# Kernel optimization log

Hardware: AMD Instinct MI355X
Metric: run time of the kernel (lower is better)

## Reference

```python
import jax, jax.numpy as jnp
import numpy as np

B, S, D, H, DFF = 8, 1024, 1024, 16, 4096
HD = D // H
EPS_COS = 1e-8
EPS_LN = 1e-5


def setup_inputs() -> dict:
    key = jax.random.key(0)
    ks = jax.random.split(key, 12)
    inp = {
        "x": jax.random.normal(ks[0], (B, S, D), jnp.float32),
        "ln1_w": jnp.ones((D,), jnp.float32),
        "ln1_b": jnp.zeros((D,), jnp.float32),
        "in_proj_w": jax.random.normal(ks[1], (3 * D, D), jnp.float32) * 0.02,
        "in_proj_b": jnp.zeros((3 * D,), jnp.float32),
        "out_proj_w": jax.random.normal(ks[2], (D, D), jnp.float32) * 0.02,
        "out_proj_b": jnp.zeros((D,), jnp.float32),
        "ln2_w": jnp.ones((D,), jnp.float32),
        "ln2_b": jnp.zeros((D,), jnp.float32),
        "mu_weight": jax.random.uniform(ks[3], (DFF, D), jnp.float32, -1.0, 1.0) * (1.0 / np.sqrt(D)),
        "sigma_weight": jax.random.normal(ks[4], (DFF, D), jnp.float32) * 0.02,
        "gate_param": jnp.full((DFF,), 0.1, jnp.float32),
        "mu_bias": jnp.zeros((DFF,), jnp.float32),
        "ffn2_w": jax.random.normal(ks[5], (D, DFF), jnp.float32) * 0.02,
        "ffn2_b": jnp.zeros((D,), jnp.float32),
    }
    return inp


def _layernorm(x, w, b):
    mu = jnp.mean(x, axis=-1, keepdims=True)
    var = jnp.mean(jnp.square(x - mu), axis=-1, keepdims=True)
    return (x - mu) * jax.lax.rsqrt(var + EPS_LN) * w + b


def _mha_causal(h, in_proj_w, in_proj_b, out_proj_w, out_proj_b):
    # h: [B,S,D]; combined qkv projection as in torch nn.MultiheadAttention
    qkv = h @ in_proj_w.T + in_proj_b                      # [B,S,3D]
    q, k, v = jnp.split(qkv, 3, axis=-1)
    def heads(t):
        return t.reshape(B, S, H, HD).transpose(0, 2, 1, 3)  # [B,H,S,HD]
    q, k, v = heads(q), heads(k), heads(v)
    logits = jnp.einsum("bhqd,bhkd->bhqk", q, k) / jnp.sqrt(jnp.float32(HD))
    causal = jnp.tril(jnp.ones((S, S), bool))
    logits = jnp.where(causal, logits, jnp.float32(-jnp.inf))
    attn = jax.nn.softmax(logits, axis=-1)
    o = jnp.einsum("bhqk,bhkd->bhqd", attn, v)
    o = o.transpose(0, 2, 1, 3).reshape(B, S, D)
    return o @ out_proj_w.T + out_proj_b


def _moie_linear(xr, mu_weight, sigma_weight, gate_param, mu_bias):
    # xr: [N,D]. cosine similarity via GEMM + norm reductions (no (N,out,in) blowup)
    keys = mu_weight * jax.nn.softplus(sigma_weight)       # [DFF,D]
    dots = xr @ keys.T                                      # [N,DFF]
    xn = jnp.maximum(jnp.linalg.norm(xr, axis=-1, keepdims=True), EPS_COS)
    kn = jnp.maximum(jnp.linalg.norm(keys, axis=-1), EPS_COS)
    scores = dots / (xn * kn[None, :])                      # [N,DFF]
    weights = jax.nn.relu(scores - gate_param[None, :])
    comp = xr @ mu_weight.T + mu_bias                       # [N,DFF]
    masked = comp * weights
    return masked, scores


def reference(x, ln1_w, ln1_b, in_proj_w, in_proj_b, out_proj_w, out_proj_b,
              ln2_w, ln2_b, mu_weight, sigma_weight, gate_param, mu_bias,
              ffn2_w, ffn2_b):
    h = _layernorm(x, ln1_w, ln1_b)
    attn_out = _mha_causal(h, in_proj_w, in_proj_b, out_proj_w, out_proj_b)
    x = x + attn_out
    ffn_in = _layernorm(x, ln2_w, ln2_b)
    xr = ffn_in.reshape(-1, D)                              # [N,D]
    masked, scores = _moie_linear(xr, mu_weight, sigma_weight, gate_param, mu_bias)
    ffn1_out = masked.reshape(B, S, DFF)
    act = jax.nn.silu(ffn1_out)
    ffn2_out = act @ ffn2_w.T + ffn2_b
    x = x + ffn2_out
    return x, scores, masked
```

## Files before the change

### kernel.cpp

```cpp
#include <hip/hip_runtime.h>

typedef unsigned short u16;
typedef unsigned int u32;
typedef unsigned long long u64;
typedef __attribute__((ext_vector_type(8))) short short8;
typedef __attribute__((ext_vector_type(4))) float f32x4;

#define DEV static __device__ __forceinline__

DEV u16 f2b(float f) {
  union { float f; u32 u; } a; a.f = f;
  u32 r = a.u + 0x7fffu + ((a.u >> 16) & 1u);
  return (u16)(r >> 16);
}

DEV f32x4 mfma16(short8 a, short8 b, f32x4 c) {
  return __builtin_amdgcn_mfma_f32_16x16x32_bf16(a, b, c, 0, 0, 0);
}

DEV void async16(const void* g, void* l) {
  __builtin_amdgcn_global_load_lds(
      (const __attribute__((address_space(1))) u32*)g,
      (__attribute__((address_space(3))) u32*)l, 16, 0, 0);
}

__global__ __launch_bounds__(256) void f2bf4(const float* __restrict__ src,
                                             u16* __restrict__ dst, int n4) {
  const int stride = gridDim.x * 256;
  for (int i = blockIdx.x * 256 + threadIdx.x; i < n4; i += stride) {
    const f32x4 v = ((const f32x4*)src)[i];
    union { u64 q; u16 s[4]; } pk;
    pk.s[0] = f2b(v[0]); pk.s[1] = f2b(v[1]); pk.s[2] = f2b(v[2]); pk.s[3] = f2b(v[3]);
    ((u64*)dst)[i] = pk.q;
  }
}

__global__ __launch_bounds__(256) void prep_keys(
    const float* __restrict__ mu, const float* __restrict__ sg,
    u16* __restrict__ wcat, float* __restrict__ kn) {
  __shared__ float s1[4];
  const int row = blockIdx.x, tid = threadIdx.x, lane = tid & 63, wave = tid >> 6;
  const f32x4 m = *(const f32x4*)(mu + (size_t)row * 1024 + tid * 4);
  const f32x4 s = *(const f32x4*)(sg + (size_t)row * 1024 + tid * 4);
  float q = 0.f;
  union { u64 q; u16 s[4]; } pkk, pkm;
  #pragma unroll
  for (int j = 0; j < 4; ++j) {
    const float sp = (s[j] > 20.f) ? s[j] : log1pf(__expf(s[j]));
    const float k = m[j] * sp;
    q += k * k;
    pkk.s[j] = f2b(k);
    pkm.s[j] = f2b(m[j]);
  }
  *(u64*)(wcat + (size_t)row * 1024 + tid * 4) = pkk.q;
  *(u64*)(wcat + (size_t)(4096 + row) * 1024 + tid * 4) = pkm.q;
  #pragma unroll
  for (int d = 1; d < 64; d <<= 1) q += __shfl_xor(q, d);
  if (lane == 0) s1[wave] = q;
  __syncthreads();
  if (tid == 0) kn[row] = 1.0f / fmaxf(sqrtf(s1[0] + s1[1] + s1[2] + s1[3]), 1e-8f);
}

__global__ __launch_bounds__(256) void ln_kernel(
    const float* __restrict__ x, const float* __restrict__ w,
    const float* __restrict__ b, u16* __restrict__ y, float* __restrict__ xn) {
  __shared__ float s1[4], s2[4];
  const int row = blockIdx.x, tid = threadIdx.x, lane = tid & 63, wave = tid >> 6;
  const f32x4 xv = *(const f32x4*)(x + (size_t)row * 1024 + tid * 4);
  float s = xv[0] + xv[1] + xv[2] + xv[3];
  float q = xv[0]*xv[0] + xv[1]*xv[1] + xv[2]*xv[2] + xv[3]*xv[3];
  #pragma unroll
  for (int d = 1; d < 64; d <<= 1) { s += __shfl_xor(s, d); q += __shfl_xor(q, d); }
  if (lane == 0) { s1[wave] = s; s2[wave] = q; }
  __syncthreads();
  s = s1[0] + s1[1] + s1[2] + s1[3];
  q = s2[0] + s2[1] + s2[2] + s2[3];
  const float mean = s * (1.f / 1024.f);
  const float inv = rsqrtf(q * (1.f / 1024.f) - mean * mean + 1e-5f);
  const f32x4 wv = *(const f32x4*)(w + tid * 4);
  const f32x4 bv = *(const f32x4*)(b + tid * 4);
  float yv[4];
  union { u64 q; u16 s[4]; } pk;
  #pragma unroll
  for (int j = 0; j < 4; ++j) {
    yv[j] = (xv[j] - mean) * inv * wv[j] + bv[j];
    pk.s[j] = f2b(yv[j]);
  }
  *(u64*)(y + (size_t)row * 1024 + tid * 4) = pk.q;
  if (xn) {
    float qs = yv[0]*yv[0] + yv[1]*yv[1] + yv[2]*yv[2] + yv[3]*yv[3];
    #pragma unroll
    for (int d = 1; d < 64; d <<= 1) qs += __shfl_xor(qs, d);
    __syncthreads();
    if (lane == 0) s1[wave] = qs;
    __syncthreads();
    if (tid == 0) xn[row] = 1.0f / fmaxf(sqrtf(s1[0] + s1[1] + s1[2] + s1[3]), 1e-8f);
  }
}

template<int MODE, int BM>
__global__ __launch_bounds__(512, 2) void gemm_bt(
    const u16* __restrict__ A, const u16* __restrict__ W,
    int M, int N, int K,
    const float* __restrict__ aux0, const float* __restrict__ aux1,
    float* __restrict__ fo0,
    u16* __restrict__ bo0, u16* __restrict__ bo1, u16* __restrict__ bo2) {
  constexpr int MF = BM / 32;
  constexpr int A_U16 = BM * 32;
  constexpr int STRIDE = A_U16 + 8192;
  constexpr int AISS = BM / 128;
  constexpr int LPT = AISS + 2;
  __shared__ __align__(16) u16 lds[3 * STRIDE];

  const int tid = threadIdx.x;
  const int lane = tid & 63, wave = tid >> 6;
  const int x = lane & 15, g = lane >> 4;
  const int wm = wave >> 2, wn = wave & 3;

  const int gx = N >> 8;
  const int nwg = gridDim.x;
  const int wg = ((int)blockIdx.x & 7) * (nwg >> 3) + ((int)blockIdx.x >> 3);
  const int by = wg / gx, bx = wg - by * gx;
  const int m0 = by * BM, n0 = bx * 256;

  const u16* srcA[AISS]; const u16* srcB[2];
  int dA[AISS], dB[2];
  #pragma unroll
  for (int i = 0; i < AISS; ++i) {
    const int rp = i * 64 + (tid >> 3);
    const int pre = (tid & 7) ^ (rp & 7);
    const int row = rp * 2 + (pre & 1), col = (pre >> 1) * 8;
    srcA[i] = A + (size_t)(m0 + row) * K + col;
    dA[i] = i * 4096 + tid * 8;
  }
  #pragma unroll
  for (int i = 0; i < 2; ++i) {
    const int rp = i * 64 + (tid >> 3);
    const int pre = (tid & 7) ^ (rp & 7);
    const int row = rp * 2 + (pre & 1), col = (pre >> 1) * 8;
    srcB[i] = W + (size_t)(n0 + row) * K + col;
    dB[i] = A_U16 + i * 4096 + tid * 8;
  }
  const int lane_off = (x >> 1) * 64 + (((2 * g + (x & 1)) ^ (x >> 1)) * 8);
  const int aoff = wm * (BM / 4) * 64 + lane_off;
  const int boff = A_U16 + wn * 2048 + lane_off;

  f32x4 acc[MF][4];
  #pragma unroll
  for (int f = 0; f < MF; ++f)
    #pragma unroll
    for (int j = 0; j < 4; ++j) acc[f][j] = (f32x4){0.f, 0.f, 0.f, 0.f};

  const int NT = K >> 5;
  auto stage = [&](int t, int b) {
    u16* buf = lds + b * STRIDE;
    const size_t ko = (size_t)t * 32;
    #pragma unroll
    for (int i = 0; i < AISS; ++i) async16(srcA[i] + ko, buf + dA[i]);
    #pragma unroll
    for (int i = 0; i < 2; ++i) async16(srcB[i] + ko, buf + dB[i]);
  };
  stage(0, 0);
  stage(1, 1);
  int br = 0, bs = 2;
  for (int t = 0; t < NT; ++t) {
    if (t < NT - 1)
      asm volatile("s_waitcnt vmcnt(%0)\n\ts_barrier" :: "n"(LPT) : "memory");
    else
      asm volatile("s_waitcnt vmcnt(0)\n\ts_barrier" ::: "memory");
    const u16* bufr = lds + br * STRIDE;
    short8 bfr[4], af[MF];
    #pragma unroll
    for (int j = 0; j < 4; ++j) bfr[j] = *(const short8*)(bufr + boff + j * 512);
    #pragma unroll
    for (int f = 0; f < MF; ++f) af[f] = *(const short8*)(bufr + aoff + f * 512);
    if (t + 2 < NT) stage(t + 2, bs);
    __builtin_amdgcn_s_setprio(1);
    #pragma unroll
    for (int f = 0; f < MF; ++f)
      #pragma unroll
      for (int j = 0; j < 4; ++j) acc[f][j] = mfma16(af[f], bfr[j], acc[f][j]);
    __builtin_amdgcn_s_setprio(0);
    br = (br == 2) ? 0 : br + 1;
    bs = (bs == 2) ? 0 : bs + 1;
  }

  const int col_base = n0 + wn * 64;
  const int row_base = m0 + wm * (BM / 2);
  #pragma unroll
  for (int f = 0; f < MF; ++f)
    #pragma unroll
    for (int j = 0; j < 4; ++j)
      #pragma unroll
      for (int r = 0; r < 4; ++r) {
        const int row = row_base + f * 16 + g * 4 + r;
        const int col = col_base + j * 16 + x;
        float v = acc[f][j][r];
        if constexpr (MODE == 0) {
          v += aux0[col];
          const int part = col >> 10, cc = col & 1023;
          const int hh = cc >> 6, dd = cc & 63;
          const size_t idx = ((size_t)((row >> 10) * 16 + hh) * 1024 + (row & 1023)) * 64 + dd;
          if (part == 0) bo0[idx] = f2b(v * 0.125f);
          else if (part == 1) bo1[idx] = f2b(v);
          else bo2[idx] = f2b(v);
        } else {
          fo0[(size_t)row * 1024 + col] = v + aux0[col] + aux1[(size_t)row * 1024 + col];
        }
      }
}

__global__ __launch_bounds__(512, 2) void gemm8p_moie(
    const u16* __restrict__ A, const u16* __restrict__ W,
    const float* __restrict__ xni, const float* __restrict__ kni,
    const float* __restrict__ mub, const float* __restrict__ gate,
    float* __restrict__ oscore, float* __restrict__ omask,
    u16* __restrict__ oact) {
  __shared__ __align__(16) u16 lds[65536];
  const int tid = threadIdx.x;
  const int lane = tid & 63, wave = tid >> 6;
  const int x = lane & 15, g = lane >> 4, h = x >> 1, pp = x & 1;
  const int wm = wave >> 2, wn = wave & 3;

  const int bid = (int)blockIdx.x;
  const int local = bid >> 3;
  const int by = (bid & 7) * 4 + (local & 3);
  const int bx = local >> 2;
  const int m0 = by * 256, n0 = bx * 128;

  const int rp0 = tid >> 3, j0 = tid & 7;
  const int prow = rp0 * 2 + (j0 & 1);
  const int pcol = (((j0 >> 1) ^ (rp0 & 3)) & 3) * 8;
  const u16* hsrc[4];
  hsrc[0] = A + (size_t)(m0 + prow) * 1024 + pcol;
  hsrc[1] = A + (size_t)(m0 + 128 + prow) * 1024 + pcol;
  hsrc[2] = W + (size_t)(n0 + prow) * 1024 + pcol;
  hsrc[3] = W + (size_t)(4096 + n0 + prow) * 1024 + pcol;
  const int dst0 = tid * 8;

  const int laneoff = h * 64 + (((2 * g + pp) ^ ((h & 3) << 1)) * 8);

  f32x4 acc[8][4];
  #pragma unroll
  for (int f = 0; f < 8; ++f)
    #pragma unroll
    for (int j = 0; j < 4; ++j) acc[f][j] = (f32x4){0.f, 0.f, 0.f, 0.f};

  auto stage = [&](int o, int kk, int kt, int b) {
    u16* dst = lds + b * 32768 + o * 16384 + kk * 8192 + dst0;
    const int koff = kt * 64 + kk * 32;
    async16(hsrc[o * 2 + 0] + koff, dst);
    async16(hsrc[o * 2 + 1] + koff, dst + 4096);
  };

  stage(1, 0, 0, 0); stage(0, 0, 0, 0); stage(1, 1, 0, 0); stage(0, 1, 0, 0);
  stage(1, 0, 1, 1); stage(0, 0, 1, 1); stage(1, 1, 1, 1);
  asm volatile("s_waitcnt vmcnt(6)\n\ts_barrier" ::: "memory");

  constexpr int NTK = 16;
  short8 bf[4];
  for (int t = 0; t < NTK; ++t) {
    const int b = t & 1;
    const u16* bufA = lds + b * 32768;
    const u16* bufB = bufA + 16384;
    #pragma unroll
    for (int w = 0; w < 4; ++w) {
      const int kk = w >> 1, fh = w & 1;
      short8 af[4];
      if (fh == 0) {
        #pragma unroll
        for (int j = 0; j < 4; ++j)
          bf[j] = *(const short8*)(bufB + kk * 8192 + wn * 2048 + j * 512 + laneoff);
      }
      #pragma unroll
      for (int f = 0; f < 4; ++f)
        af[f] = *(const short8*)(bufA + kk * 8192 + wm * 4096 + (fh * 4 + f) * 512 + laneoff);
      if (w == 0) { if (t + 1 < NTK) stage(0, 1, t + 1, (t + 1) & 1); }
      else if (t + 2 < NTK) {
        if (w == 1) stage(1, 0, t + 2, b);
        else if (w == 2) stage(0, 0, t + 2, b);
        else stage(1, 1, t + 2, b);
      }
      asm volatile("s_barrier" ::: "memory");
      asm volatile("s_waitcnt lgkmcnt(0)" ::: "memory");
      __builtin_amdgcn_sched_barrier(0);
      __builtin_amdgcn_s_setprio(1);
      #pragma unroll
      for (int f = 0; f < 4; ++f)
        #pragma unroll
        for (int j = 0; j < 4; ++j)
          acc[fh * 4 + f][j] = mfma16(af[f], bf[j], acc[fh * 4 + f][j]);
      __builtin_amdgcn_s_setprio(0);
      if (w == 3 && t + 1 < NTK) {
        if (t + 1 < NTK - 1)
          asm volatile("s_waitcnt vmcnt(6)\n\ts_barrier" ::: "memory");
        else
          asm volatile("s_waitcnt vmcnt(0)\n\ts_barrier" ::: "memory");
      } else {
        asm volatile("s_barrier" ::: "memory");
      }
    }
  }

  __syncthreads();
  float* sl = (float*)lds;
  if (wn < 2) {
    #pragma unroll
    for (int f = 0; f < 8; ++f)
      #pragma unroll
      for (int j = 0; j < 4; ++j) {
        const int lcol = wn * 64 + j * 16 + x;
        const int gcol = n0 + lcol;
        const float kv = kni[gcol];
        #pragma unroll
        for (int r = 0; r < 4; ++r) {
          const int lrow = wm * 128 + f * 16 + g * 4 + r;
          const int grow = m0 + lrow;
          const float s = acc[f][j][r] * xni[grow] * kv;
          sl[lrow * 128 + (lcol ^ (g << 4))] = s;
          oscore[(size_t)grow * 4096 + gcol] = s;
        }
      }
  }
  __syncthreads();
  if (wn >= 2) {
    #pragma unroll
    for (int f = 0; f < 8; ++f)
      #pragma unroll
      for (int j = 0; j < 4; ++j) {
        const int lcol = (wn - 2) * 64 + j * 16 + x;
        const int gcol = n0 + lcol;
        const float gt = gate[gcol], mb = mub[gcol];
        #pragma unroll
        for (int r = 0; r < 4; ++r) {
          const int lrow = wm * 128 + f * 16 + g * 4 + r;
          const int grow = m0 + lrow;
          const float s = sl[lrow * 128 + (lcol ^ (g << 4))];
          const float comp = acc[f][j][r] + mb;
          const float mk = comp * fmaxf(s - gt, 0.f);
          omask[(size_t)grow * 4096 + gcol] = mk;
          oact[(size_t)grow * 4096 + gcol] = f2b(mk / (1.f + __expf(-mk)));
        }
      }
  }
}

__global__ __launch_bounds__(256) void attn_kernel(
    const u16* __restrict__ Q, const u16* __restrict__ Kg,
    const u16* __restrict__ Vg, u16* __restrict__ O) {
  __shared__ __align__(16) u16 Kl[64 * 72];
  __shared__ __align__(16) u16 Vt[64 * 72];
  __shared__ __align__(16) u16 Pl[4][16 * 72];
  const int bh = blockIdx.x;
  const int qt = blockIdx.y;
  const int tid = threadIdx.x, lane = tid & 63, wave = tid >> 6;
  const int x = lane & 15, g = lane >> 4;
  const u16* Qb = Q + (size_t)bh * 1024 * 64;
  const u16* Kb = Kg + (size_t)bh * 1024 * 64;
  const u16* Vb = Vg + (size_t)bh * 1024 * 64;
  const int qbase = qt * 64 + wave * 16;
  const short8 qf0 = *(const short8*)&Qb[(qbase + x) * 64 + g * 8];
  const short8 qf1 = *(const short8*)&Qb[(qbase + x) * 64 + 32 + g * 8];
  float mrun[4], lrun[4];
  f32x4 oacc[4];
  #pragma unroll
  for (int r = 0; r < 4; ++r) { mrun[r] = -1e30f; lrun[r] = 0.f; }
  #pragma unroll
  for (int d = 0; d < 4; ++d) oacc[d] = (f32x4){0.f, 0.f, 0.f, 0.f};

  for (int t = 0; t <= qt; ++t) {
    __syncthreads();
    #pragma unroll
    for (int p = 0; p < 2; ++p) {
      const int s = tid + p * 256;
      const int row = s >> 3, c = s & 7;
      *(short8*)&Kl[row * 72 + c * 8] = *(const short8*)&Kb[(size_t)(t * 64 + row) * 64 + c * 8];
    }
    #pragma unroll
    for (int p = 0; p < 2; ++p) {
      const int kv = (tid >> 3) + p * 32;
      const int d0 = (tid & 7) * 8;
      const short8 v8 = *(const short8*)&Vb[(size_t)(t * 64 + kv) * 64 + d0];
      #pragma unroll
      for (int j = 0; j < 8; ++j) {
        const int d = d0 + j;
        Vt[d * 72 + ((kv + 8 * ((d >> 3) & 7)) & 63)] = (u16)v8[j];
      }
    }
    __syncthreads();

    float sc[4][4];
    #pragma unroll
    for (int nb = 0; nb < 4; ++nb) {
      f32x4 a = (f32x4){0.f, 0.f, 0.f, 0.f};
      const short8 kf0 = *(const short8*)&Kl[(nb * 16 + x) * 72 + g * 8];
      const short8 kf1 = *(const short8*)&Kl[(nb * 16 + x) * 72 + 32 + g * 8];
      a = mfma16(qf0, kf0, a);
      a = mfma16(qf1, kf1, a);
      #pragma unroll
      for (int r = 0; r < 4; ++r) sc[nb][r] = a[r];
    }
    if (t == qt) {
      #pragma unroll
      for (int nb = 0; nb < 4; ++nb)
        #pragma unroll
        for (int r = 0; r < 4; ++r)
          if (t * 64 + nb * 16 + x > qbase + g * 4 + r) sc[nb][r] = -1e30f;
    }
    float mnew[4], psum[4], scl[4];
    #pragma unroll
    for (int r = 0; r < 4; ++r) {
      float mx = fmaxf(fmaxf(sc[0][r], sc[1][r]), fmaxf(sc[2][r], sc[3][r]));
      #pragma unroll
      for (int d = 1; d < 16; d <<= 1) mx = fmaxf(mx, __shfl_xor(mx, d));
      mnew[r] = fmaxf(mrun[r], mx);
      scl[r] = __expf(mrun[r] - mnew[r]);
      mrun[r] = mnew[r];
      psum[r] = 0.f;
    }
    float p[4][4];
    #pragma unroll
    for (int nb = 0; nb < 4; ++nb)
      #pragma unroll
      for (int r = 0; r < 4; ++r) {
        p[nb][r] = __expf(sc[nb][r] - mnew[r]);
        psum[r] += p[nb][r];
      }
    #pragma unroll
    for (int r = 0; r < 4; ++r) {
      #pragma unroll
      for (int d = 1; d < 16; d <<= 1) psum[r] += __shfl_xor(psum[r], d);
      lrun[r] = lrun[r] * scl[r] + psum[r];
      #pragma unroll
      for (int db = 0; db < 4; ++db) oacc[db][r] *= scl[r];
    }
    u16* Pw = Pl[wave];
    #pragma unroll
    for (int nb = 0; nb < 4; ++nb)
      #pragma unroll
      for (int r = 0; r < 4; ++r)
        Pw[(g * 4 + r) * 72 + nb * 16 + x] = f2b(p[nb][r]);
    const short8 pf0 = *(const short8*)&Pw[x * 72 + g * 8];
    const short8 pf1 = *(const short8*)&Pw[x * 72 + 32 + g * 8];
    #pragma unroll
    for (int db = 0; db < 4; ++db) {
      const int d = db * 16 + x;
      const int swz = 8 * ((d >> 3) & 7);
      const short8 vf0 = *(const short8*)&Vt[d * 72 + ((g * 8 + swz) & 63)];
      const short8 vf1 = *(const short8*)&Vt[d * 72 + ((g * 8 + 32 + swz) & 63)];
      oacc[db] = mfma16(pf0, vf0, oacc[db]);
      oacc[db] = mfma16(pf1, vf1, oacc[db]);
    }
  }
  const int b = bh >> 4, hh = bh & 15;
  #pragma unroll
  for (int db = 0; db < 4; ++db)
    #pragma unroll
    for (int r = 0; r < 4; ++r) {
      const int qrow = qbase + g * 4 + r;
      O[((size_t)(b * 1024 + qrow)) * 1024 + hh * 64 + db * 16 + x] = f2b(oacc[db][r] / lrun[r]);
    }
}

extern "C" void kernel_launch(void* const* d_in, const int* in_sizes, int n_in,
                              void* d_out, int out_size, void* d_ws, size_t ws_size,
                              hipStream_t stream) {
  const float* x    = (const float*)d_in[0];
  const float* ln1w = (const float*)d_in[1];
  const float* ln1b = (const float*)d_in[2];
  const float* wip  = (const float*)d_in[3];
  const float* bip  = (const float*)d_in[4];
  const float* wop  = (const float*)d_in[5];
  const float* bop  = (const float*)d_in[6];
  const float* ln2w = (const float*)d_in[7];
  const float* ln2b = (const float*)d_in[8];
  const float* muw  = (const float*)d_in[9];
  const float* sgw  = (const float*)d_in[10];
  const float* gate = (const float*)d_in[11];
  const float* mub  = (const float*)d_in[12];
  const float* wf2  = (const float*)d_in[13];
  const float* bf2  = (const float*)d_in[14];

  float* out_x = (float*)d_out;
  float* out_scores = out_x + (size_t)8192 * 1024;
  float* out_masked = out_scores + (size_t)8192 * 4096;

  char* ws = (char*)d_ws;
  size_t off = 0;
  auto alloc = [&](size_t n) { char* p = ws + off; off += (n + 255) & ~(size_t)255; return p; };
  u16* h_bf    = (u16*)alloc((size_t)8192 * 1024 * 2);
  u16* q_bf    = (u16*)alloc((size_t)8192 * 1024 * 2);
  u16* k_bf    = (u16*)alloc((size_t)8192 * 1024 * 2);
  u16* v_bf    = (u16*)alloc((size_t)8192 * 1024 * 2);
  u16* o_bf    = (u16*)alloc((size_t)8192 * 1024 * 2);
  float* x_res = (float*)alloc((size_t)8192 * 1024 * 4);
  u16* xr_bf   = (u16*)alloc((size_t)8192 * 1024 * 2);
  float* xn    = (float*)alloc((size_t)8192 * 4);
  float* kn    = (float*)alloc((size_t)4096 * 4);
  u16* wcat    = (u16*)alloc((size_t)8192 * 1024 * 2);
  u16* wip_b   = (u16*)alloc((size_t)3072 * 1024 * 2);
  u16* wop_b   = (u16*)alloc((size_t)1024 * 1024 * 2);
  u16* wf2_b   = (u16*)alloc((size_t)1024 * 4096 * 2);
  u16* act_bf  = (u16*)alloc((size_t)8192 * 4096 * 2);

  f2bf4<<<1024, 256, 0, stream>>>(wip, wip_b, 3072 * 1024 / 4);
  f2bf4<<<512, 256, 0, stream>>>(wop, wop_b, 1024 * 1024 / 4);
  f2bf4<<<1024, 256, 0, stream>>>(wf2, wf2_b, 1024 * 4096 / 4);
  prep_keys<<<4096, 256, 0, stream>>>(muw, sgw, wcat, kn);
  ln_kernel<<<8192, 256, 0, stream>>>(x, ln1w, ln1b, h_bf, nullptr);
  gemm_bt<0, 256><<<384, 512, 0, stream>>>(h_bf, wip_b, 8192, 3072, 1024,
      bip, nullptr, nullptr, q_bf, k_bf, v_bf);
  attn_kernel<<<dim3(128, 16), 256, 0, stream>>>(q_bf, k_bf, v_bf, o_bf);
  gemm_bt<1, 128><<<256, 512, 0, stream>>>(o_bf, wop_b, 8192, 1024, 1024,
      bop, x, x_res, nullptr, nullptr, nullptr);
  ln_kernel<<<8192, 256, 0, stream>>>(x_res, ln2w, ln2b, xr_bf, xn);
  gemm8p_moie<<<1024, 512, 0, stream>>>(xr_bf, wcat, xn, kn, mub, gate,
      out_scores, out_masked, act_bf);
  gemm_bt<3, 128><<<256, 512, 0, stream>>>(act_bf, wf2_b, 8192, 1024, 4096,
      bf2, x_res, out_x, nullptr, nullptr, nullptr);
}
```

Before: 598.2 us.

## Interleave key/mu weight rows per wave and deepen MOIE GEMM pipeline

The fused MOIE GEMM now loads B rows so that key and mu_weight rows for the same output column sit in the same wave's fragments: each 64-row chunk holds 32 key rows followed by 32 mu rows. This lets every wave compute score, mask and SiLU directly from its own registers, removing the LDS round trip and the two __syncthreads in the epilogue. The K loop also moves from a 2-buffer, 64-wide stage to a 4-buffer, 32-wide stage ring with three stages in flight, which adds barriers per k-step but gives more latency hiding.

```diff
diff --git a/kernel.cpp b/kernel.cpp
--- a/kernel.cpp
+++ b/kernel.cpp
@@ -210,13 +210,13 @@
       }
 }
 
-__global__ __launch_bounds__(512, 2) void gemm8p_moie(
+__global__ __launch_bounds__(512, 2) void moie_gemm(
     const u16* __restrict__ A, const u16* __restrict__ W,
     const float* __restrict__ xni, const float* __restrict__ kni,
     const float* __restrict__ mub, const float* __restrict__ gate,
     float* __restrict__ oscore, float* __restrict__ omask,
     u16* __restrict__ oact) {
-  __shared__ __align__(16) u16 lds[65536];
+  __shared__ __align__(16) u16 lds[4 * 16384];
   const int tid = threadIdx.x;
   const int lane = tid & 63, wave = tid >> 6;
   const int x = lane & 15, g = lane >> 4, h = x >> 1, pp = x & 1;
@@ -231,117 +231,96 @@
   const int rp0 = tid >> 3, j0 = tid & 7;
   const int prow = rp0 * 2 + (j0 & 1);
   const int pcol = (((j0 >> 1) ^ (rp0 & 3)) & 3) * 8;
-  const u16* hsrc[4];
-  hsrc[0] = A + (size_t)(m0 + prow) * 1024 + pcol;
-  hsrc[1] = A + (size_t)(m0 + 128 + prow) * 1024 + pcol;
-  hsrc[2] = W + (size_t)(n0 + prow) * 1024 + pcol;
-  hsrc[3] = W + (size_t)(4096 + n0 + prow) * 1024 + pcol;
+  const u16* Asrc[2]; const u16* Bsrc[2];
+  Asrc[0] = A + (size_t)(m0 + prow) * 1024 + pcol;
+  Asrc[1] = A + (size_t)(m0 + 128 + prow) * 1024 + pcol;
+  #pragma unroll
+  for (int c = 0; c < 2; ++c) {
+    const int rb = c * 128 + prow;
+    const u16* base = (rb & 32) ? (W + (size_t)4096 * 1024) : W;
+    Bsrc[c] = base + (size_t)(n0 + ((rb >> 6) << 5) + (rb & 31)) * 1024 + pcol;
+  }
   const int dst0 = tid * 8;
-
   const int laneoff = h * 64 + (((2 * g + pp) ^ ((h & 3) << 1)) * 8);
 
   f32x4 acc[8][4];
   #pragma unroll
-  for (int f = 0; f < 8; ++f)
-    #pragma unroll
-    for (int j = 0; j < 4; ++j) acc[f][j] = (f32x4){0.f, 0.f, 0.f, 0.f};
-
-  auto stage = [&](int o, int kk, int kt, int b) {
-    u16* dst = lds + b * 32768 + o * 16384 + kk * 8192 + dst0;
-    const int koff = kt * 64 + kk * 32;
-    async16(hsrc[o * 2 + 0] + koff, dst);
-    async16(hsrc[o * 2 + 1] + koff, dst + 4096);
+  for (int i = 0; i < 8; ++i)
+    #pragma unroll
+    for (int j = 0; j < 4; ++j) acc[i][j] = (f32x4){0.f, 0.f, 0.f, 0.f};
+
+  auto stageA = [&](int t) {
+    u16* dst = lds + (t & 3) * 16384 + dst0;
+    const int ko = t * 32;
+    async16(Asrc[0] + ko, dst);
+    async16(Asrc[1] + ko, dst + 4096);
   };
-
-  stage(1, 0, 0, 0); stage(0, 0, 0, 0); stage(1, 1, 0, 0); stage(0, 1, 0, 0);
-  stage(1, 0, 1, 1); stage(0, 0, 1, 1); stage(1, 1, 1, 1);
-  asm volatile("s_waitcnt vmcnt(6)\n\ts_barrier" ::: "memory");
-
-  constexpr int NTK = 16;
-  short8 bf[4];
-  for (int t = 0; t < NTK; ++t) {
-    const int b = t & 1;
-    const u16* bufA = lds + b * 32768;
-    const u16* bufB = bufA + 16384;
-    #pragma unroll
-    for (int w = 0; w < 4; ++w) {
-      const int kk = w >> 1, fh = w & 1;
-      short8 af[4];
-      if (fh == 0) {
-        #pragma unroll
-        for (int j = 0; j < 4; ++j)
-          bf[j] = *(const short8*)(bufB + kk * 8192 + wn * 2048 + j * 512 + laneoff);
+  auto stageB = [&](int t) {
+    u16* dst = lds + (t & 3) * 16384 + 8192 + dst0;
+    const int ko = t * 32;
+    async16(Bsrc[0] + ko, dst);
+    async16(Bsrc[1] + ko, dst + 4096);
+  };
+
+  stageA(0); stageB(0); stageA(1); stageB(1); stageA(2); stageB(2);
+  asm volatile("s_waitcnt vmcnt(8)\n\ts_barrier" ::: "memory");
+
+  constexpr int NT = 32;
+  for (int t = 0; t < NT; ++t) {
+    const u16* bufA = lds + (t & 3) * 16384;
+    const u16* bufB = bufA + 8192;
+    short8 bf[4], af[4];
+    #pragma unroll
+    for (int j = 0; j < 4; ++j) bf[j] = *(const short8*)(bufB + wn * 2048 + j * 512 + laneoff);
+    #pragma unroll
+    for (int f = 0; f < 4; ++f) af[f] = *(const short8*)(bufA + wm * 4096 + f * 512 + laneoff);
+    if (t + 3 < NT) stageB(t + 3);
+    asm volatile("s_barrier" ::: "memory");
+    asm volatile("s_waitcnt lgkmcnt(0)" ::: "memory");
+    __builtin_amdgcn_s_setprio(1);
+    #pragma unroll
+    for (int f = 0; f < 4; ++f)
+      #pragma unroll
+      for (int j = 0; j < 4; ++j) acc[f][j] = mfma16(af[f], bf[j], acc[f][j]);
+    __builtin_amdgcn_s_setprio(0);
+    asm volatile("s_barrier" ::: "memory");
+    #pragma unroll
+    for (int f = 0; f < 4; ++f) af[f] = *(const short8*)(bufA + wm * 4096 + (4 + f) * 512 + laneoff);
+    if (t + 3 < NT) stageA(t + 3);
+    asm volatile("s_barrier" ::: "memory");
+    asm volatile("s_waitcnt lgkmcnt(0)" ::: "memory");
+    __builtin_amdgcn_s_setprio(1);
+    #pragma unroll
+    for (int f = 0; f < 4; ++f)
+      #pragma unroll
+      for (int j = 0; j < 4; ++j) acc[4 + f][j] = mfma16(af[f], bf[j], acc[4 + f][j]);
+    __builtin_amdgcn_s_setprio(0);
+    if (t <= NT - 4)
+      asm volatile("s_waitcnt vmcnt(8)\n\ts_barrier" ::: "memory");
+    else if (t == NT - 3)
+      asm volatile("s_waitcnt vmcnt(4)\n\ts_barrier" ::: "memory");
+    else if (t == NT - 2)
+      asm volatile("s_waitcnt vmcnt(0)\n\ts_barrier" ::: "memory");
+  }
+
+  #pragma unroll
+  for (int i = 0; i < 8; ++i) {
+    const int row = m0 + wm * 128 + i * 16 + g * 4;
+    const f32x4 xv = *(const f32x4*)(xni + row);
+    #pragma unroll
+    for (int jj = 0; jj < 2; ++jj) {
+      const int gcol = n0 + wn * 32 + jj * 16 + x;
+      const float kv = kni[gcol], gt = gate[gcol], mb = mub[gcol];
+      #pragma unroll
+      for (int r = 0; r < 4; ++r) {
+        const float s = acc[i][jj][r] * xv[r] * kv;
+        const float comp = acc[i][jj + 2][r] + mb;
+        const float mk = comp * fmaxf(s - gt, 0.f);
+        oscore[(size_t)(row + r) * 4096 + gcol] = s;
+        omask[(size_t)(row + r) * 4096 + gcol] = mk;
+        oact[(size_t)(row + r) * 4096 + gcol] = f2b(mk / (1.f + __expf(-mk)));
       }
-      #pragma unroll
-      for (int f = 0; f < 4; ++f)
-        af[f] = *(const short8*)(bufA + kk * 8192 + wm * 4096 + (fh * 4 + f) * 512 + laneoff);
-      if (w == 0) { if (t + 1 < NTK) stage(0, 1, t + 1, (t + 1) & 1); }
-      else if (t + 2 < NTK) {
-        if (w == 1) stage(1, 0, t + 2, b);
-        else if (w == 2) stage(0, 0, t + 2, b);
-        else stage(1, 1, t + 2, b);
-      }
-      asm volatile("s_barrier" ::: "memory");
-      asm volatile("s_waitcnt lgkmcnt(0)" ::: "memory");
-      __builtin_amdgcn_sched_barrier(0);
-      __builtin_amdgcn_s_setprio(1);
-      #pragma unroll
-      for (int f = 0; f < 4; ++f)
-        #pragma unroll
-        for (int j = 0; j < 4; ++j)
-          acc[fh * 4 + f][j] = mfma16(af[f], bf[j], acc[fh * 4 + f][j]);
-      __builtin_amdgcn_s_setprio(0);
-      if (w == 3 && t + 1 < NTK) {
-        if (t + 1 < NTK - 1)
-          asm volatile("s_waitcnt vmcnt(6)\n\ts_barrier" ::: "memory");
-        else
-          asm volatile("s_waitcnt vmcnt(0)\n\ts_barrier" ::: "memory");
-      } else {
-        asm volatile("s_barrier" ::: "memory");
-      }
-    }
-  }
-
-  __syncthreads();
-  float* sl = (float*)lds;
-  if (wn < 2) {
-    #pragma unroll
-    for (int f = 0; f < 8; ++f)
-      #pragma unroll
-      for (int j = 0; j < 4; ++j) {
-        const int lcol = wn * 64 + j * 16 + x;
-        const int gcol = n0 + lcol;
-        const float kv = kni[gcol];
-        #pragma unroll
-        for (int r = 0; r < 4; ++r) {
-          const int lrow = wm * 128 + f * 16 + g * 4 + r;
-          const int grow = m0 + lrow;
-          const float s = acc[f][j][r] * xni[grow] * kv;
-          sl[lrow * 128 + (lcol ^ (g << 4))] = s;
-          oscore[(size_t)grow * 4096 + gcol] = s;
-        }
-      }
-  }
-  __syncthreads();
-  if (wn >= 2) {
-    #pragma unroll
-    for (int f = 0; f < 8; ++f)
-      #pragma unroll
-      for (int j = 0; j < 4; ++j) {
-        const int lcol = (wn - 2) * 64 + j * 16 + x;
-        const int gcol = n0 + lcol;
-        const float gt = gate[gcol], mb = mub[gcol];
-        #pragma unroll
-        for (int r = 0; r < 4; ++r) {
-          const int lrow = wm * 128 + f * 16 + g * 4 + r;
-          const int grow = m0 + lrow;
-          const float s = sl[lrow * 128 + (lcol ^ (g << 4))];
-          const float comp = acc[f][j][r] + mb;
-          const float mk = comp * fmaxf(s - gt, 0.f);
-          omask[(size_t)grow * 4096 + gcol] = mk;
-          oact[(size_t)grow * 4096 + gcol] = f2b(mk / (1.f + __expf(-mk)));
-        }
-      }
+    }
   }
 }
 
@@ -514,7 +493,7 @@
   gemm_bt<1, 128><<<256, 512, 0, stream>>>(o_bf, wop_b, 8192, 1024, 1024,
       bop, x, x_res, nullptr, nullptr, nullptr);
   ln_kernel<<<8192, 256, 0, stream>>>(x_res, ln2w, ln2b, xr_bf, xn);
-  gemm8p_moie<<<1024, 512, 0, stream>>>(xr_bf, wcat, xn, kn, mub, gate,
+  moie_gemm<<<1024, 512, 0, stream>>>(xr_bf, wcat, xn, kn, mub, gate,
       out_scores, out_masked, act_bf);
   gemm_bt<3, 128><<<256, 512, 0, stream>>>(act_bf, wf2_b, 8192, 1024, 4096,
       bf2, x_res, out_x, nullptr, nullptr, nullptr);
```

New measurement: 541.7 us. 9.4% less time.
